# Optimization experiments

Measured on AMD Instinct MI355X. Metric: run time of the kernel, lower is better.

The kernel has to match this reference:

```python
import jax, jax.numpy as jnp
import numpy as np

B, S, D = 8, 2048, 128

def setup_inputs() -> dict:
    key = jax.random.key(0)
    kq, kk, kv = jax.random.split(key, 3)
    return {
        "Q": jax.random.normal(kq, (B, S, D), dtype=jnp.float32),
        "K": jax.random.normal(kk, (B, S, D), dtype=jnp.float32),
        "V": jax.random.normal(kv, (B, S, D), dtype=jnp.float32),
    }

def reference(Q, K, V):
    dim = Q.shape[-1]
    scores = jnp.einsum('bqd,bkd->bqk', Q, K) / jnp.sqrt(jnp.float32(dim))
    seq_len = Q.shape[1]
    # causal mask: -inf above the diagonal (matches torch.triu(ones*-inf, diagonal=1))
    causal = jnp.triu(jnp.full((seq_len, seq_len), -jnp.inf, dtype=scores.dtype), k=1)
    scores = scores + causal
    weights = jax.nn.softmax(scores, axis=-1)
    context = jnp.einsum('bqk,bkd->bqd', weights, V)
    return context
```

## Files before the change

### kernel.cpp

```cpp
#include <hip/hip_runtime.h>

#define B_ 8
#define S_ 2048
#define D_ 128
#define NT_ 64
#define FRAG_ 512

typedef __attribute__((ext_vector_type(4))) float f32x4;
typedef __attribute__((ext_vector_type(16))) float f32x16;
typedef __attribute__((ext_vector_type(8))) short bf16x8;
typedef __attribute__((ext_vector_type(4))) unsigned u32x4;
typedef __attribute__((ext_vector_type(2))) unsigned uint32x2;

#define MF(a, b, c) __builtin_amdgcn_mfma_f32_32x32x16_bf16(a, b, c, 0, 0, 0)

__device__ __forceinline__ short f2bf(float f) {
  union { float f; unsigned u; } x; x.f = f;
  unsigned r = x.u + 0x7FFFu + ((x.u >> 16) & 1u);
  return (short)(r >> 16);
}

__device__ __forceinline__ float exp2_hw(float x) {
  float r;
  asm("v_exp_f32 %0, %1" : "=v"(r) : "v"(x));
  return r;
}

__device__ __forceinline__ unsigned cvt_pk_bf16(float lo, float hi) {
  unsigned r;
  asm("v_cvt_pk_bf16_f32 %0, %1, %2" : "=v"(r) : "v"(lo), "v"(hi));
  return r;
}

__device__ __forceinline__ void plswap(unsigned& a, unsigned& b, int hi) {
#if __has_builtin(__builtin_amdgcn_permlane32_swap)
  uint32x2 r = __builtin_amdgcn_permlane32_swap(a, b, false, false);
  a = r[0]; b = r[1];
#else
  unsigned pa = (unsigned)__shfl_xor((int)a, 32, 64);
  unsigned pb = (unsigned)__shfl_xor((int)b, 32, 64);
  unsigned na = hi ? pb : a;
  unsigned nb = hi ? b : pa;
  a = na; b = nb;
#endif
}

__device__ __forceinline__ f32x16 zero16() {
  f32x16 v = {0.f,0.f,0.f,0.f,0.f,0.f,0.f,0.f,0.f,0.f,0.f,0.f,0.f,0.f,0.f,0.f};
  return v;
}

__global__ __launch_bounds__(256) void prep_frag(
    const float* __restrict__ Q, const float* __restrict__ K,
    const float* __restrict__ V, short* __restrict__ Qf,
    short* __restrict__ Kf, short* __restrict__ Vf) {
  __shared__ short qt[32][136], kt[32][136], vt[32][136];
  const int b  = blockIdx.x & 7;
  const int st = blockIdx.x >> 3;
  const int t  = threadIdx.x;
  const int row = t >> 3, c0 = (t & 7) * 16;
  const size_t base = ((size_t)(b * S_ + st * 32 + row)) * D_ + c0;
  const float scq = 0.12751744553939605f;

  #pragma unroll
  for (int i = 0; i < 4; ++i) {
    f32x4 q = *(const f32x4*)(Q + base + i * 4);
    f32x4 k = *(const f32x4*)(K + base + i * 4);
    f32x4 v = *(const f32x4*)(V + base + i * 4);
    #pragma unroll
    for (int j = 0; j < 4; ++j) {
      qt[row][c0 + i * 4 + j] = f2bf(q[j] * scq);
      kt[row][c0 + i * 4 + j] = f2bf(k[j]);
      vt[row][c0 + i * 4 + j] = f2bf(v[j]);
    }
  }
  __syncthreads();

  const int l = t & 63, ln = l & 31, hi = l >> 5, w = t >> 6;
  const size_t gidx = (size_t)(b * NT_ + st) * 8;
  #pragma unroll
  for (int i = 0; i < 2; ++i) {
    const int m = w * 2 + i;
    bf16x8 qv = *(const bf16x8*)&qt[ln][m * 16 + hi * 8];
    bf16x8 kv = *(const bf16x8*)&kt[ln][m * 16 + hi * 8];
    *(bf16x8*)(Qf + (gidx + m) * FRAG_ + l * 8) = qv;
    *(bf16x8*)(Kf + (gidx + m) * FRAG_ + l * 8) = kv;
    const int d4 = m >> 1, h = m & 1;
    bf16x8 vv;
    #pragma unroll
    for (int j = 0; j < 8; ++j) vv[j] = vt[h * 16 + hi * 8 + j][d4 * 32 + ln];
    *(bf16x8*)(Vf + (gidx + m) * FRAG_ + l * 8) = vv;
  }
}

__global__ __launch_bounds__(512, 2) void fattn_fwd(
    const short* __restrict__ Qf, const short* __restrict__ Kf,
    const short* __restrict__ Vf, float* __restrict__ Og) {
  const int task = blockIdx.x;
  const int j    = task >> 3;
  const int b    = task & 7;
  const int tid  = threadIdx.x;
  const int w    = __builtin_amdgcn_readfirstlane(tid >> 6);
  const int lane = tid & 63;
  const int ln   = lane & 31;
  const int hi   = lane >> 5;
  const int lane8 = lane * 8;

  const short* Qfb = Qf + (size_t)b * (NT_ * 8 * FRAG_);
  const short* Kfb = Kf + (size_t)b * (NT_ * 8 * FRAG_);
  const short* Vfb = Vf + (size_t)b * (NT_ * 8 * FRAG_);
  float*       Ob  = Og + (size_t)b * S_ * D_;

  __shared__ float ldsO[4][4][32][33];
  __shared__ float lS[8][32], invLS[32];

  #pragma unroll 1
  for (int phase = 0; phase < 2; ++phase) {
    const int tt = phase ? (63 - j) : j;
    const int q0 = tt * 32;

    bf16x8 qb[8];
    {
      const short* qfp = Qfb + (size_t)tt * (8 * FRAG_);
      #pragma unroll
      for (int dt = 0; dt < 8; ++dt)
        qb[dt] = *(const bf16x8*)(qfp + dt * FRAG_ + lane8);
    }

    f32x16 o[4];
    #pragma unroll
    for (int i = 0; i < 4; ++i) o[i] = zero16();
    float l_part = 0.f;

    int s = w;
    if (s <= tt) {
      bf16x8 kb[8];
      {
        const short* kfp = Kfb + (size_t)s * (8 * FRAG_);
        #pragma unroll
        for (int dt = 0; dt < 8; ++dt)
          kb[dt] = *(const bf16x8*)(kfp + dt * FRAG_ + lane8);
      }

      for (;;) {
        const short* vfp = Vfb + (size_t)s * (8 * FRAG_);
        bf16x8 va[8];
        #pragma unroll
        for (int m8 = 0; m8 < 8; ++m8)
          va[m8] = *(const bf16x8*)(vfp + m8 * FRAG_ + lane8);

        f32x16 sv = zero16();
        __builtin_amdgcn_s_setprio(1);
        #pragma unroll
        for (int dt = 0; dt < 8; ++dt) sv = MF(kb[dt], qb[dt], sv);
        __builtin_amdgcn_s_setprio(0);

        const bool lastst = (s + 8 > tt);
        if (!lastst) {
          const short* k2 = Kfb + (size_t)(s + 8) * (8 * FRAG_);
          #pragma unroll
          for (int dt = 0; dt < 8; ++dt)
            kb[dt] = *(const bf16x8*)(k2 + dt * FRAG_ + lane8);
        }

        if (s == tt) {
          #pragma unroll
          for (int r = 0; r < 16; ++r) {
            const int kl = (r & 3) + 8 * (r >> 2) + 4 * hi;
            if (kl > ln) sv[r] = -512.0f;
          }
        }

        float p[16];
        #pragma unroll
        for (int r = 0; r < 16; ++r) p[r] = exp2_hw(sv[r]);
        float ts[8];
        #pragma unroll
        for (int r = 0; r < 8; ++r) ts[r] = p[r] + p[r + 8];
        #pragma unroll
        for (int r = 0; r < 4; ++r) ts[r] = ts[r] + ts[r + 4];
        l_part += (ts[0] + ts[1]) + (ts[2] + ts[3]);

        unsigned x0 = cvt_pk_bf16(p[0], p[1]),  x1 = cvt_pk_bf16(p[2], p[3]);
        unsigned y0 = cvt_pk_bf16(p[4], p[5]),  y1 = cvt_pk_bf16(p[6], p[7]);
        plswap(x0, y0, hi); plswap(x1, y1, hi);
        unsigned z0 = cvt_pk_bf16(p[8], p[9]),  z1 = cvt_pk_bf16(p[10], p[11]);
        unsigned w0 = cvt_pk_bf16(p[12], p[13]), w1 = cvt_pk_bf16(p[14], p[15]);
        plswap(z0, w0, hi); plswap(z1, w1, hi);
        u32x4 t0 = {x0, x1, y0, y1};
        u32x4 t1 = {z0, z1, w0, w1};
        bf16x8 pb0 = __builtin_bit_cast(bf16x8, t0);
        bf16x8 pb1 = __builtin_bit_cast(bf16x8, t1);

        __builtin_amdgcn_s_setprio(1);
        #pragma unroll
        for (int d4 = 0; d4 < 4; ++d4) {
          o[d4] = MF(va[d4 * 2],     pb0, o[d4]);
          o[d4] = MF(va[d4 * 2 + 1], pb1, o[d4]);
        }
        __builtin_amdgcn_s_setprio(0);

        if (lastst) break;
        s += 8;
      }
    }

    float l = l_part + __shfl_xor(l_part, 32, 64);
    if (hi == 0) lS[w][ln] = l;

    if (w < 4) {
      #pragma unroll
      for (int d4 = 0; d4 < 4; ++d4)
        #pragma unroll
        for (int r = 0; r < 16; ++r)
          ldsO[w][d4][ln][(r & 3) + 8 * (r >> 2) + 4 * hi] = o[d4][r];
    }
    __syncthreads();

    if (tid < 32) {
      float L = lS[0][tid];
      #pragma unroll
      for (int w2 = 1; w2 < 8; ++w2) L += lS[w2][tid];
      invLS[tid] = 1.0f / L;
    }

    float oacc[8];
    #pragma unroll
    for (int k = 0; k < 8; ++k) {
      const int e = k * 512 + tid;
      const int row = e >> 7;
      const int col = e & 127;
      float acc = 0.f;
      #pragma unroll
      for (int w2 = 0; w2 < 4; ++w2)
        acc += ldsO[w2][col >> 5][row][col & 31];
      oacc[k] = acc;
    }
    __syncthreads();

    if (w >= 4) {
      #pragma unroll
      for (int d4 = 0; d4 < 4; ++d4)
        #pragma unroll
        for (int r = 0; r < 16; ++r)
          ldsO[w - 4][d4][ln][(r & 3) + 8 * (r >> 2) + 4 * hi] = o[d4][r];
    }
    __syncthreads();

    #pragma unroll
    for (int k = 0; k < 8; ++k) {
      const int e = k * 512 + tid;
      const int row = e >> 7;
      const int col = e & 127;
      float acc = oacc[k];
      #pragma unroll
      for (int w2 = 0; w2 < 4; ++w2)
        acc += ldsO[w2][col >> 5][row][col & 31];
      Ob[(size_t)(q0 + row) * D_ + col] = acc * invLS[row];
    }
    __syncthreads();
  }
}

extern "C" void kernel_launch(void* const* d_in, const int* in_sizes, int n_in,
                              void* d_out, int out_size, void* d_ws, size_t ws_size,
                              hipStream_t stream) {
  const float* Q = (const float*)d_in[0];
  const float* K = (const float*)d_in[1];
  const float* V = (const float*)d_in[2];
  float* O = (float*)d_out;

  short* Qf = (short*)d_ws;
  short* Kf = Qf + (size_t)B_ * S_ * D_;
  short* Vf = Kf + (size_t)B_ * S_ * D_;

  prep_frag<<<B_ * NT_, 256, 0, stream>>>(Q, K, V, Qf, Kf, Vf);
  fattn_fwd<<<B_ * 32, 512, 0, stream>>>(Qf, Kf, Vf, O);
}
```

Measured before the change: 28.11 us.

## Assign two adjacent query tiles per block with four KV-split waves each

Each block now handles two consecutive 32-row query tiles at once, with four waves per tile splitting the KV range in stride 4. Before, all eight waves worked on one tile at a time across two phases, pairing tile j with tile 63-j for load balance. Blocks are dispatched heaviest-first (i = 31 - idx/8) and the launch bound drops the min-blocks hint. The goal is to remove the serial two-phase loop and its barriers, at the cost of uneven per-block work that relies on the reversed dispatch order to balance.

```diff
diff --git a/kernel.cpp b/kernel.cpp
--- a/kernel.cpp
+++ b/kernel.cpp
@@ -93,14 +93,17 @@
   }
 }
 
-__global__ __launch_bounds__(512, 2) void fattn_fwd(
+__global__ __launch_bounds__(512) void fattn_fwd(
     const short* __restrict__ Qf, const short* __restrict__ Kf,
     const short* __restrict__ Vf, float* __restrict__ Og) {
-  const int task = blockIdx.x;
-  const int j    = task >> 3;
-  const int b    = task & 7;
+  const int idx  = blockIdx.x;
+  const int i    = 31 - (idx >> 3);
+  const int b    = idx & 7;
   const int tid  = threadIdx.x;
   const int w    = __builtin_amdgcn_readfirstlane(tid >> 6);
+  const int sub  = w >> 2;
+  const int kv   = w & 3;
+  const int tt   = 2 * i + sub;
   const int lane = tid & 63;
   const int ln   = lane & 31;
   const int hi   = lane >> 5;
@@ -114,152 +117,136 @@
   __shared__ float ldsO[4][4][32][33];
   __shared__ float lS[8][32], invLS[32];
 
-  #pragma unroll 1
-  for (int phase = 0; phase < 2; ++phase) {
-    const int tt = phase ? (63 - j) : j;
-    const int q0 = tt * 32;
-
-    bf16x8 qb[8];
+  bf16x8 qb[8];
+  {
+    const short* qfp = Qfb + (size_t)tt * (8 * FRAG_);
+    #pragma unroll
+    for (int dt = 0; dt < 8; ++dt)
+      qb[dt] = *(const bf16x8*)(qfp + dt * FRAG_ + lane8);
+  }
+
+  f32x16 o[4];
+  #pragma unroll
+  for (int q = 0; q < 4; ++q) o[q] = zero16();
+  float l_part = 0.f;
+
+  int s = kv;
+  if (s <= tt) {
+    bf16x8 kb[8];
     {
-      const short* qfp = Qfb + (size_t)tt * (8 * FRAG_);
+      const short* kfp = Kfb + (size_t)s * (8 * FRAG_);
       #pragma unroll
       for (int dt = 0; dt < 8; ++dt)
-        qb[dt] = *(const bf16x8*)(qfp + dt * FRAG_ + lane8);
+        kb[dt] = *(const bf16x8*)(kfp + dt * FRAG_ + lane8);
     }
 
-    f32x16 o[4];
-    #pragma unroll
-    for (int i = 0; i < 4; ++i) o[i] = zero16();
-    float l_part = 0.f;
-
-    int s = w;
-    if (s <= tt) {
-      bf16x8 kb[8];
-      {
-        const short* kfp = Kfb + (size_t)s * (8 * FRAG_);
+    for (;;) {
+      const short* vfp = Vfb + (size_t)s * (8 * FRAG_);
+      bf16x8 va[8];
+      #pragma unroll
+      for (int m8 = 0; m8 < 8; ++m8)
+        va[m8] = *(const bf16x8*)(vfp + m8 * FRAG_ + lane8);
+
+      f32x16 sv = zero16();
+      __builtin_amdgcn_s_setprio(1);
+      #pragma unroll
+      for (int dt = 0; dt < 8; ++dt) sv = MF(kb[dt], qb[dt], sv);
+      __builtin_amdgcn_s_setprio(0);
+
+      const bool lastst = (s + 4 > tt);
+      if (!lastst) {
+        const short* k2 = Kfb + (size_t)(s + 4) * (8 * FRAG_);
         #pragma unroll
         for (int dt = 0; dt < 8; ++dt)
-          kb[dt] = *(const bf16x8*)(kfp + dt * FRAG_ + lane8);
+          kb[dt] = *(const bf16x8*)(k2 + dt * FRAG_ + lane8);
       }
 
-      for (;;) {
-        const short* vfp = Vfb + (size_t)s * (8 * FRAG_);
-        bf16x8 va[8];
+      if (s == tt) {
         #pragma unroll
-        for (int m8 = 0; m8 < 8; ++m8)
-          va[m8] = *(const bf16x8*)(vfp + m8 * FRAG_ + lane8);
-
-        f32x16 sv = zero16();
-        __builtin_amdgcn_s_setprio(1);
-        #pragma unroll
-        for (int dt = 0; dt < 8; ++dt) sv = MF(kb[dt], qb[dt], sv);
-        __builtin_amdgcn_s_setprio(0);
-
-        const bool lastst = (s + 8 > tt);
-        if (!lastst) {
-          const short* k2 = Kfb + (size_t)(s + 8) * (8 * FRAG_);
-          #pragma unroll
-          for (int dt = 0; dt < 8; ++dt)
-            kb[dt] = *(const bf16x8*)(k2 + dt * FRAG_ + lane8);
+        for (int r = 0; r < 16; ++r) {
+          const int kl = (r & 3) + 8 * (r >> 2) + 4 * hi;
+          if (kl > ln) sv[r] = -512.0f;
         }
-
-        if (s == tt) {
-          #pragma unroll
-          for (int r = 0; r < 16; ++r) {
-            const int kl = (r & 3) + 8 * (r >> 2) + 4 * hi;
-            if (kl > ln) sv[r] = -512.0f;
-          }
-        }
-
-        float p[16];
-        #pragma unroll
-        for (int r = 0; r < 16; ++r) p[r] = exp2_hw(sv[r]);
-        float ts[8];
-        #pragma unroll
-        for (int r = 0; r < 8; ++r) ts[r] = p[r] + p[r + 8];
-        #pragma unroll
-        for (int r = 0; r < 4; ++r) ts[r] = ts[r] + ts[r + 4];
-        l_part += (ts[0] + ts[1]) + (ts[2] + ts[3]);
-
-        unsigned x0 = cvt_pk_bf16(p[0], p[1]),  x1 = cvt_pk_bf16(p[2], p[3]);
-        unsigned y0 = cvt_pk_bf16(p[4], p[5]),  y1 = cvt_pk_bf16(p[6], p[7]);
-        plswap(x0, y0, hi); plswap(x1, y1, hi);
-        unsigned z0 = cvt_pk_bf16(p[8], p[9]),  z1 = cvt_pk_bf16(p[10], p[11]);
-        unsigned w0 = cvt_pk_bf16(p[12], p[13]), w1 = cvt_pk_bf16(p[14], p[15]);
-        plswap(z0, w0, hi); plswap(z1, w1, hi);
-        u32x4 t0 = {x0, x1, y0, y1};
-        u32x4 t1 = {z0, z1, w0, w1};
-        bf16x8 pb0 = __builtin_bit_cast(bf16x8, t0);
-        bf16x8 pb1 = __builtin_bit_cast(bf16x8, t1);
-
-        __builtin_amdgcn_s_setprio(1);
-        #pragma unroll
-        for (int d4 = 0; d4 < 4; ++d4) {
-          o[d4] = MF(va[d4 * 2],     pb0, o[d4]);
-          o[d4] = MF(va[d4 * 2 + 1], pb1, o[d4]);
-        }
-        __builtin_amdgcn_s_setprio(0);
-
-        if (lastst) break;
-        s += 8;
       }
+
+      float p[16];
+      #pragma unroll
+      for (int r = 0; r < 16; ++r) p[r] = exp2_hw(sv[r]);
+      float ts[8];
+      #pragma unroll
+      for (int r = 0; r < 8; ++r) ts[r] = p[r] + p[r + 8];
+      #pragma unroll
+      for (int r = 0; r < 4; ++r) ts[r] = ts[r] + ts[r + 4];
+      l_part += (ts[0] + ts[1]) + (ts[2] + ts[3]);
+
+      unsigned x0 = cvt_pk_bf16(p[0], p[1]),  x1 = cvt_pk_bf16(p[2], p[3]);
+      unsigned y0 = cvt_pk_bf16(p[4], p[5]),  y1 = cvt_pk_bf16(p[6], p[7]);
+      plswap(x0, y0, hi); plswap(x1, y1, hi);
+      unsigned z0 = cvt_pk_bf16(p[8], p[9]),  z1 = cvt_pk_bf16(p[10], p[11]);
+      unsigned w0 = cvt_pk_bf16(p[12], p[13]), w1 = cvt_pk_bf16(p[14], p[15]);
+      plswap(z0, w0, hi); plswap(z1, w1, hi);
+      u32x4 t0 = {x0, x1, y0, y1};
+      u32x4 t1 = {z0, z1, w0, w1};
+      bf16x8 pb0 = __builtin_bit_cast(bf16x8, t0);
+      bf16x8 pb1 = __builtin_bit_cast(bf16x8, t1);
+
+      __builtin_amdgcn_s_setprio(1);
+      #pragma unroll
+      for (int d4 = 0; d4 < 4; ++d4) {
+        o[d4] = MF(va[d4 * 2],     pb0, o[d4]);
+        o[d4] = MF(va[d4 * 2 + 1], pb1, o[d4]);
+      }
+      __builtin_amdgcn_s_setprio(0);
+
+      if (lastst) break;
+      s += 4;
     }
-
-    float l = l_part + __shfl_xor(l_part, 32, 64);
-    if (hi == 0) lS[w][ln] = l;
-
-    if (w < 4) {
-      #pragma unroll
-      for (int d4 = 0; d4 < 4; ++d4)
-        #pragma unroll
-        for (int r = 0; r < 16; ++r)
-          ldsO[w][d4][ln][(r & 3) + 8 * (r >> 2) + 4 * hi] = o[d4][r];
-    }
-    __syncthreads();
-
-    if (tid < 32) {
-      float L = lS[0][tid];
-      #pragma unroll
-      for (int w2 = 1; w2 < 8; ++w2) L += lS[w2][tid];
-      invLS[tid] = 1.0f / L;
-    }
-
-    float oacc[8];
-    #pragma unroll
-    for (int k = 0; k < 8; ++k) {
-      const int e = k * 512 + tid;
-      const int row = e >> 7;
-      const int col = e & 127;
-      float acc = 0.f;
-      #pragma unroll
-      for (int w2 = 0; w2 < 4; ++w2)
-        acc += ldsO[w2][col >> 5][row][col & 31];
-      oacc[k] = acc;
-    }
-    __syncthreads();
-
-    if (w >= 4) {
-      #pragma unroll
-      for (int d4 = 0; d4 < 4; ++d4)
-        #pragma unroll
-        for (int r = 0; r < 16; ++r)
-          ldsO[w - 4][d4][ln][(r & 3) + 8 * (r >> 2) + 4 * hi] = o[d4][r];
-    }
-    __syncthreads();
-
-    #pragma unroll
-    for (int k = 0; k < 8; ++k) {
-      const int e = k * 512 + tid;
-      const int row = e >> 7;
-      const int col = e & 127;
-      float acc = oacc[k];
-      #pragma unroll
-      for (int w2 = 0; w2 < 4; ++w2)
-        acc += ldsO[w2][col >> 5][row][col & 31];
-      Ob[(size_t)(q0 + row) * D_ + col] = acc * invLS[row];
-    }
-    __syncthreads();
-  }
+  }
+
+  float l2 = l_part + __shfl_xor(l_part, 32, 64);
+  if (hi == 0) lS[w][ln] = l2;
+
+#define WRITE_O()                                                        \
+  do {                                                                   \
+    _Pragma("unroll")                                                    \
+    for (int d4 = 0; d4 < 4; ++d4)                                       \
+      _Pragma("unroll")                                                  \
+      for (int r = 0; r < 16; ++r)                                       \
+        ldsO[kv][d4][ln][(r & 3) + 8 * (r >> 2) + 4 * hi] = o[d4][r];    \
+  } while (0)
+
+#define MERGE_WRITE(q0_)                                                 \
+  do {                                                                   \
+    _Pragma("unroll")                                                    \
+    for (int k = 0; k < 8; ++k) {                                        \
+      const int e = k * 512 + tid;                                       \
+      const int row = e >> 7;                                            \
+      const int col = e & 127;                                           \
+      float acc = ldsO[0][col >> 5][row][col & 31]                       \
+                + ldsO[1][col >> 5][row][col & 31]                       \
+                + ldsO[2][col >> 5][row][col & 31]                       \
+                + ldsO[3][col >> 5][row][col & 31];                      \
+      Ob[(size_t)((q0_) + row) * D_ + col] = acc * invLS[row];           \
+    }                                                                    \
+  } while (0)
+
+  if (sub == 0) WRITE_O();
+  __syncthreads();
+  if (tid < 32)
+    invLS[tid] = 1.0f / (lS[0][tid] + lS[1][tid] + lS[2][tid] + lS[3][tid]);
+  __syncthreads();
+  MERGE_WRITE(64 * i);
+  __syncthreads();
+
+  if (sub == 1) WRITE_O();
+  __syncthreads();
+  if (tid < 32)
+    invLS[tid] = 1.0f / (lS[4][tid] + lS[5][tid] + lS[6][tid] + lS[7][tid]);
+  __syncthreads();
+  MERGE_WRITE(64 * i + 32);
+
+#undef WRITE_O
+#undef MERGE_WRITE
 }
 
 extern "C" void kernel_launch(void* const* d_in, const int* in_sizes, int n_in,
```

Result: slower. 33.89 us (+20.6%).
